# Optimization experiments

Measured on AMD Instinct MI355X. Metric: run time of the kernel, lower is better.

The kernel has to match this reference:

```python
import jax, jax.numpy as jnp
import numpy as np

# dims: E ensemble, F feature channels, O = num_objs+1 nodes, B batch
E, F, O, B, DIN = 4, 16, 9, 512, 32
H, DK = 4, 32          # num_heads, attn_dim per head
DH = 128               # feature_fc / attn_out / post_fc hidden dim
FINAL = F + 1          # final_size = feature_dim + 1


def _lin(x, w, b=None):
    # per-ensemble, per-channel, per-object batched linear:
    # x: [E,F,O,B,i], w: [E,F,O,i,j], b: [E,F,O,1,j]
    y = jnp.einsum('efobi,efoij->efobj', x, w)
    return y if b is None else y + b


def _channel_mha(x, wq, wk, wv, wo, pw, pb):
    # Channel multi-head attention over the O object nodes, per (E,F) channel.
    e, f, o, b, _ = x.shape
    heads = lambda t: t.reshape(e, f, o, b, H, DK)
    q = heads(_lin(x, wq))
    k = heads(_lin(x, wk))
    v = heads(_lin(x, wv))
    scale = jnp.asarray(1.0 / np.sqrt(DK), x.dtype)
    logits = jnp.einsum('efqbhd,efkbhd->efbhqk', q, k) * scale  # [E,F,B,H,O,O]
    attn = jax.nn.softmax(logits, axis=-1)
    out = jnp.einsum('efbhqk,efkbhd->efqbhd', attn, v).reshape(e, f, o, b, H * DK)
    out = _lin(out, wo) + x                 # output projection + residual
    return jax.nn.relu(_lin(out, pw, pb))   # post_fc (post_fc_dims=[DH])


def setup_inputs() -> dict:
    key = jax.random.key(0)
    ks = jax.random.split(key, 32)
    W = lambda k, shape, fan_in: (jax.random.normal(k, shape, jnp.float32)
                                  / np.sqrt(fan_in).astype(np.float32))
    inp = {}
    inp['x'] = jax.random.normal(ks[0], (E, F, O, B, DIN), jnp.float32)
    inp['fw1'] = W(ks[1], (E, F, O, DIN, DH), DIN)
    inp['fb1'] = jnp.zeros((E, F, O, 1, DH), jnp.float32)
    inp['fw2'] = W(ks[2], (E, F, O, DH, DH), DH)
    inp['fb2'] = jnp.zeros((E, F, O, 1, DH), jnp.float32)
    idx = 3
    for i in range(2):
        for n in ('wq', 'wk', 'wv', 'wo', 'pw'):
            inp[f'a{i}_{n}'] = W(ks[idx], (E, F, O, DH, DH), DH)
            idx += 1
        inp[f'a{i}_pb'] = jnp.zeros((E, F, O, 1, DH), jnp.float32)
    inp['pw1'] = W(ks[idx], (E, F, DH, DH), DH); idx += 1
    inp['pb1'] = jnp.zeros((E, F, 1, DH), jnp.float32)
    inp['pw2'] = W(ks[idx], (E, F, DH, FINAL), DH)
    inp['pb2'] = jnp.zeros((E, F, 1, FINAL), jnp.float32)
    return inp


def reference(x, fw1, fb1, fw2, fb2,
              a0_wq, a0_wk, a0_wv, a0_wo, a0_pw, a0_pb,
              a1_wq, a1_wk, a1_wv, a1_wo, a1_pw, a1_pb,
              pw1, pb1, pw2, pb2):
    # sa_feature per-object MLP (feature_fc_dims = [128, 128])
    h = jax.nn.relu(_lin(x, fw1, fb1))
    h = jax.nn.relu(_lin(h, fw2, fb2))
    # num_attns = 2 ChannelMHAttention blocks over object nodes
    h = _channel_mha(h, a0_wq, a0_wk, a0_wv, a0_wo, a0_pw, a0_pb)
    h = _channel_mha(h, a1_wq, a1_wk, a1_wv, a1_wo, a1_pw, a1_pb)
    # pool over object axis (predictor weights have no object dim)
    pooled = h.mean(axis=2)  # [E,F,B,DH]
    p = jax.nn.relu(jnp.einsum('efbi,efij->efbj', pooled, pw1) + pb1)
    return jnp.einsum('efbi,efij->efbj', p, pw2) + pb2  # [E,F,B,F+1]
```

## Files before the change

### kernel.cpp

```cpp
#include <hip/hip_runtime.h>
#include <hip/hip_bf16.h>

typedef __bf16 bvec8 __attribute__((ext_vector_type(8)));
typedef __bf16 bvec4 __attribute__((ext_vector_type(4)));
typedef float fvec4 __attribute__((ext_vector_type(4)));

#define E_ 4
#define F_ 16
#define O_ 9
#define B_ 512
#define DIN_ 32
#define H_ 4
#define DK_ 32
#define DH_ 128
#define FINAL_ 17
#define EF_ 64
#define EFO_ 576

__global__ __launch_bounds__(256) void transpose_k(const float* __restrict__ in,
                                                   __bf16* __restrict__ out, int R, int C) {
  __shared__ float tile[64 * 65];
  int r0 = blockIdx.y * 64, c0 = blockIdx.x * 64;
  const float* src = in + (size_t)blockIdx.z * R * C;
  __bf16* dst = out + (size_t)blockIdx.z * R * C;
  for (int idx = threadIdx.x; idx < 4096; idx += 256) {
    int r = idx >> 6, c = idx & 63;
    if ((r0 + r) < R && (c0 + c) < C)
      tile[r * 65 + c] = src[(size_t)(r0 + r) * C + (c0 + c)];
  }
  __syncthreads();
  for (int idx = threadIdx.x; idx < 4096; idx += 256) {
    int c = idx >> 6, r = idx & 63;
    if ((r0 + r) < R && (c0 + c) < C)
      dst[(size_t)(c0 + c) * R + (r0 + r)] = (__bf16)tile[r * 65 + c];
  }
}

__global__ __launch_bounds__(256) void transpose3_k(const float* __restrict__ i0,
    const float* __restrict__ i1, const float* __restrict__ i2,
    __bf16* __restrict__ o0, __bf16* __restrict__ o1, __bf16* __restrict__ o2) {
  __shared__ float tile[64 * 65];
  int z = blockIdx.z;
  int which = z / EFO_, zb = z - which * EFO_;
  const float* in = which == 0 ? i0 : (which == 1 ? i1 : i2);
  __bf16* out = which == 0 ? o0 : (which == 1 ? o1 : o2);
  int r0 = blockIdx.y * 64, c0 = blockIdx.x * 64;
  const float* src = in + (size_t)zb * DH_ * DH_;
  __bf16* dst = out + (size_t)zb * DH_ * DH_;
  for (int idx = threadIdx.x; idx < 4096; idx += 256) {
    int r = idx >> 6, c = idx & 63;
    tile[r * 65 + c] = src[(size_t)(r0 + r) * DH_ + (c0 + c)];
  }
  __syncthreads();
  for (int idx = threadIdx.x; idx < 4096; idx += 256) {
    int c = idx >> 6, r = idx & 63;
    dst[(size_t)(c0 + c) * DH_ + (r0 + r)] = (__bf16)tile[r * 65 + c];
  }
}

__global__ __launch_bounds__(256) void transpose2_k(const float* __restrict__ i0,
    const float* __restrict__ i1, __bf16* __restrict__ o0, __bf16* __restrict__ o1) {
  __shared__ float tile[64 * 65];
  int z = blockIdx.z;
  int which = z / EFO_, zb = z - which * EFO_;
  const float* in = which == 0 ? i0 : i1;
  __bf16* out = which == 0 ? o0 : o1;
  int r0 = blockIdx.y * 64, c0 = blockIdx.x * 64;
  const float* src = in + (size_t)zb * DH_ * DH_;
  __bf16* dst = out + (size_t)zb * DH_ * DH_;
  for (int idx = threadIdx.x; idx < 4096; idx += 256) {
    int r = idx >> 6, c = idx & 63;
    tile[r * 65 + c] = src[(size_t)(r0 + r) * DH_ + (c0 + c)];
  }
  __syncthreads();
  for (int idx = threadIdx.x; idx < 4096; idx += 256) {
    int c = idx >> 6, r = idx & 63;
    dst[(size_t)(c0 + c) * DH_ + (r0 + r)] = (__bf16)tile[r * 65 + c];
  }
}


__device__ __forceinline__ void stage_async(const __bf16* __restrict__ g, int ldg,
                                            __bf16* s, int cols) {
  int lane = threadIdx.x & 63, w = threadIdx.x >> 6;
  int nwb = cols >> 2;
  for (int wb = w; wb < nwb; wb += 8) {
    int p = wb >> 3, r0 = (wb & 7) << 4;
    int r = r0 + (lane >> 2), c = lane & 3;
    const __bf16* gp = g + (size_t)r * ldg + p * 32 + c * 8;
    __bf16* lp = s + (((p << 7) + r0) << 5);
    __builtin_amdgcn_global_load_lds((const __attribute__((address_space(1))) void*)gp,
                                     (__attribute__((address_space(3))) void*)lp,
                                     16, 0, 0);
  }
}

__device__ __forceinline__ void stage_tile_f32_512(const float* __restrict__ g, int ldg,
                                                   __bf16* s, int cols) {
  int cpr = cols >> 3;
  int nch = 128 * cpr;
  for (int c = threadIdx.x; c < nch; c += 512) {
    int r = c / cpr;
    int cc = (c - r * cpr) << 3;
    const float* gp = g + (size_t)r * ldg + cc;
    float4 f0 = *(const float4*)gp;
    float4 f1 = *(const float4*)(gp + 4);
    bvec8 bv;
    bv[0] = (__bf16)f0.x; bv[1] = (__bf16)f0.y; bv[2] = (__bf16)f0.z; bv[3] = (__bf16)f0.w;
    bv[4] = (__bf16)f1.x; bv[5] = (__bf16)f1.y; bv[6] = (__bf16)f1.z; bv[7] = (__bf16)f1.w;
    *(bvec8*)(s + ((cc >> 5) * 128 + r) * 32 + (cc & 31)) = bv;
  }
}

__device__ __forceinline__ void stage_tile(const __bf16* __restrict__ g, int ldg,
                                           __bf16* s, int cols) {
  int cpr = cols >> 3;
  int nch = 128 * cpr;
  for (int c = threadIdx.x; c < nch; c += 256) {
    int r = c / cpr;
    int cc = (c - r * cpr) << 3;
    *(uint4*)(s + ((cc >> 5) * 128 + r) * 32 + (cc & 31)) =
        *(const uint4*)(g + (size_t)r * ldg + cc);
  }
}

__device__ __forceinline__ void gemm128_8(const __bf16* Ms, const __bf16* Ns, int K,
                                          fvec4 acc[4][2], int wm, int wn, int lm, int q8) {
  for (int k0 = 0; k0 < K; k0 += 32) {
    const __bf16* ap = Ms + (k0 >> 5) * 4096 + q8;
    const __bf16* bp = Ns + (k0 >> 5) * 4096 + q8;
    bvec8 a[4], b[2];
#pragma unroll
    for (int i = 0; i < 4; i++) a[i] = *(const bvec8*)(ap + (wm + i * 16 + lm) * 32);
#pragma unroll
    for (int j = 0; j < 2; j++) b[j] = *(const bvec8*)(bp + (wn + j * 16 + lm) * 32);
#pragma unroll
    for (int i = 0; i < 4; i++)
#pragma unroll
      for (int j = 0; j < 2; j++)
        acc[i][j] = __builtin_amdgcn_mfma_f32_16x16x32_bf16(a[i], b[j], acc[i][j], 0, 0, 0);
  }
}

__device__ __forceinline__ void gemm128(const __bf16* As, const __bf16* Ws, int K,
                                        fvec4 acc[4][4], int wm, int wn, int lm, int q8) {
  for (int k0 = 0; k0 < K; k0 += 32) {
    const __bf16* ap = As + (k0 >> 5) * 4096 + q8;
    const __bf16* bp = Ws + (k0 >> 5) * 4096 + q8;
    bvec8 a[4], b[4];
#pragma unroll
    for (int i = 0; i < 4; i++) a[i] = *(const bvec8*)(ap + (wm + i * 16 + lm) * 32);
#pragma unroll
    for (int j = 0; j < 4; j++) b[j] = *(const bvec8*)(bp + (wn + j * 16 + lm) * 32);
#pragma unroll
    for (int i = 0; i < 4; i++)
#pragma unroll
      for (int j = 0; j < 4; j++)
        acc[i][j] = __builtin_amdgcn_mfma_f32_16x16x32_bf16(a[i], b[j], acc[i][j], 0, 0, 0);
  }
}

__global__ __launch_bounds__(512) void mlp_kernel(const float* __restrict__ x,
    const __bf16* __restrict__ fw1t, const float* __restrict__ fb1,
    const __bf16* __restrict__ fw2t, const float* __restrict__ fb2,
    __bf16* __restrict__ h0) {
  __shared__ __align__(16) __bf16 smem[32768];
  int efo = blockIdx.y, mt = blockIdx.x;
  int t = threadIdx.x, l = t & 63, w = t >> 6;
  int wm = (w & 1) * 64, wn = (w >> 1) * 32;
  int lm = l & 15, q8 = (l >> 4) * 8, qr = (l >> 4) * 4;
  __bf16* xs = smem;
  __bf16* w1s = smem + 4096;
  __bf16* h1s = smem;
  __bf16* w2s = smem + 16384;
  stage_async(fw2t + (size_t)efo * DH_ * DH_, DH_, w2s, DH_);
  stage_async(fw1t + (size_t)efo * DH_ * DIN_, DIN_, w1s, DIN_);
  stage_tile_f32_512(x + ((size_t)efo * B_ + mt * 128) * DIN_, DIN_, xs, DIN_);
  __syncthreads();
  fvec4 zero4 = {0.f, 0.f, 0.f, 0.f};
  fvec4 acc[4][2];
#pragma unroll
  for (int i = 0; i < 4; i++)
#pragma unroll
    for (int j = 0; j < 2; j++) acc[i][j] = zero4;
  gemm128_8(w1s, xs, 32, acc, wm, wn, lm, q8);
  __syncthreads();
#pragma unroll
  for (int i = 0; i < 4; i++) {
    float4 b4 = *(const float4*)(fb1 + efo * DH_ + wm + i * 16 + qr);
    float br[4] = {b4.x, b4.y, b4.z, b4.w};
#pragma unroll
    for (int j = 0; j < 2; j++) {
      int wc0 = wm + i * 16 + qr, bb = wn + j * 16 + lm;
      bvec4 pk;
#pragma unroll
      for (int r = 0; r < 4; r++) pk[r] = (__bf16)fmaxf(acc[i][j][r] + br[r], 0.f);
      *(bvec4*)(h1s + ((wc0 >> 5) * 128 + bb) * 32 + (wc0 & 31)) = pk;
    }
  }
  __syncthreads();
#pragma unroll
  for (int i = 0; i < 4; i++)
#pragma unroll
    for (int j = 0; j < 2; j++) acc[i][j] = zero4;
  gemm128_8(w2s, h1s, 128, acc, wm, wn, lm, q8);
#pragma unroll
  for (int i = 0; i < 4; i++) {
    float4 b4 = *(const float4*)(fb2 + efo * DH_ + wm + i * 16 + qr);
    float br[4] = {b4.x, b4.y, b4.z, b4.w};
#pragma unroll
    for (int j = 0; j < 2; j++) {
      int wc0 = wm + i * 16 + qr, bb = wn + j * 16 + lm;
      bvec4 pk;
#pragma unroll
      for (int r = 0; r < 4; r++) pk[r] = (__bf16)fmaxf(acc[i][j][r] + br[r], 0.f);
      *(bvec4*)(h0 + ((size_t)efo * B_ + mt * 128 + bb) * DH_ + wc0) = pk;
    }
  }
}

__global__ __launch_bounds__(512) void qkv_kernel(const __bf16* __restrict__ hsrc,
    const __bf16* __restrict__ wqt, const __bf16* __restrict__ wkt,
    const __bf16* __restrict__ wvt, __bf16* __restrict__ qdst,
    __bf16* __restrict__ kdst, __bf16* __restrict__ vdst) {
  __shared__ __align__(16) __bf16 smem[32768];
  int efo = blockIdx.y, mt = blockIdx.x;
  int ef = efo / O_, o = efo - ef * O_;
  int t = threadIdx.x, l = t & 63, w = t >> 6;
  int wm = (w & 1) * 64, wn = (w >> 1) * 32;
  int lm = l & 15, q8 = (l >> 4) * 8, qr = (l >> 4) * 4;
  __bf16* hs = smem;
  __bf16* wsm = smem + 16384;
  stage_async(hsrc + ((size_t)efo * B_ + mt * 128) * DH_, DH_, hs, DH_);
  stage_async(wqt + (size_t)efo * DH_ * DH_, DH_, wsm, DH_);
  fvec4 zero4 = {0.f, 0.f, 0.f, 0.f};
  fvec4 acc[4][2];
  auto zero_acc = [&]() {
#pragma unroll
    for (int i = 0; i < 4; i++)
#pragma unroll
      for (int j = 0; j < 2; j++) acc[i][j] = zero4;
  };
  auto store_head = [&](__bf16* __restrict__ dst) {
#pragma unroll
    for (int i = 0; i < 4; i++)
#pragma unroll
      for (int j = 0; j < 2; j++) {
        int wc0 = wm + i * 16 + qr, bb = wn + j * 16 + lm;
        bvec4 pk;
#pragma unroll
        for (int r = 0; r < 4; r++) pk[r] = (__bf16)acc[i][j][r];
        *(bvec4*)(dst + ((((size_t)ef * H_ + (wc0 >> 5)) * O_ + o) * B_ +
                         mt * 128 + bb) * DK_ + (wc0 & 31)) = pk;
      }
  };
  __syncthreads();
  zero_acc();
  gemm128_8(wsm, hs, 128, acc, wm, wn, lm, q8);
  __syncthreads();
  stage_async(wkt + (size_t)efo * DH_ * DH_, DH_, wsm, DH_);
  store_head(qdst);
  __syncthreads();
  zero_acc();
  gemm128_8(wsm, hs, 128, acc, wm, wn, lm, q8);
  __syncthreads();
  stage_async(wvt + (size_t)efo * DH_ * DH_, DH_, wsm, DH_);
  store_head(kdst);
  __syncthreads();
  zero_acc();
  gemm128_8(wsm, hs, 128, acc, wm, wn, lm, q8);
  store_head(vdst);
}

__global__ __launch_bounds__(256) void attn_kernel(const __bf16* __restrict__ q,
    __bf16* kv, const __bf16* __restrict__ v) {
  int t = threadIdx.x;
  int g = t >> 2, sub = t & 3;
  int blk = blockIdx.x;
  int bt = blk & 7, efh = blk >> 3;
  int b = bt * 64 + g, d0 = sub * 8;
  size_t base = (size_t)efh * O_ * B_ * DK_ + (size_t)b * DK_ + d0;
  const size_t ostr = (size_t)B_ * DK_;
  bvec8 kr[9], vr[9];
#pragma unroll
  for (int o = 0; o < 9; o++) kr[o] = *(const bvec8*)(kv + base + (size_t)o * ostr);
#pragma unroll
  for (int o = 0; o < 9; o++) vr[o] = *(const bvec8*)(v + base + (size_t)o * ostr);
  const float scale = 0.17677669529663687f;
#pragma unroll 1
  for (int oq = 0; oq < 9; oq++) {
    bvec8 qv = *(const bvec8*)(q + base + (size_t)oq * ostr);
    float qf[8];
#pragma unroll
    for (int j = 0; j < 8; j++) qf[j] = (float)qv[j];
    float lg[9];
#pragma unroll
    for (int ok = 0; ok < 9; ok++) {
      float s = 0.f;
#pragma unroll
      for (int j = 0; j < 8; j++) s += qf[j] * (float)kr[ok][j];
      s += __shfl_xor(s, 1);
      s += __shfl_xor(s, 2);
      lg[ok] = s * scale;
    }
    float mx = lg[0];
#pragma unroll
    for (int ok = 1; ok < 9; ok++) mx = fmaxf(mx, lg[ok]);
    float sum = 0.f;
#pragma unroll
    for (int ok = 0; ok < 9; ok++) { lg[ok] = __expf(lg[ok] - mx); sum += lg[ok]; }
    float inv = 1.f / sum;
    float oacc[8] = {0.f, 0.f, 0.f, 0.f, 0.f, 0.f, 0.f, 0.f};
#pragma unroll
    for (int ok = 0; ok < 9; ok++)
#pragma unroll
      for (int j = 0; j < 8; j++) oacc[j] += lg[ok] * (float)vr[ok][j];
    bvec8 ov;
#pragma unroll
    for (int j = 0; j < 8; j++) ov[j] = (__bf16)(oacc[j] * inv);
    *(bvec8*)(kv + base + (size_t)oq * ostr) = ov;
  }
}

__global__ __launch_bounds__(512) void proj_kernel(const __bf16* __restrict__ ain,
    const __bf16* __restrict__ wot, const __bf16* __restrict__ pwt,
    const float* __restrict__ pb, const __bf16* resid,
    __bf16* hout) {
  __shared__ __align__(16) __bf16 smem[32768];
  int efo = blockIdx.y, mt = blockIdx.x;
  int ef = efo / O_, o = efo - ef * O_;
  int t = threadIdx.x, l = t & 63, w = t >> 6;
  int wm = (w & 1) * 64, wn = (w >> 1) * 32;
  int lm = l & 15, q8 = (l >> 4) * 8, qr = (l >> 4) * 4;
  __bf16* as2 = smem;
  __bf16* wsm = smem + 16384;
#pragma unroll
  for (int hh = 0; hh < 4; hh++)
    stage_async(ain + ((((size_t)ef * H_ + hh) * O_ + o) * B_ + mt * 128) * DK_, DK_,
                as2 + hh * 4096, DK_);
  stage_async(wot + (size_t)efo * DH_ * DH_, DH_, wsm, DH_);
  __syncthreads();
  fvec4 zero4 = {0.f, 0.f, 0.f, 0.f};
  fvec4 acc[4][2];
#pragma unroll
  for (int i = 0; i < 4; i++)
#pragma unroll
    for (int j = 0; j < 2; j++) acc[i][j] = zero4;
  gemm128_8(wsm, as2, 128, acc, wm, wn, lm, q8);
#pragma unroll
  for (int i = 0; i < 4; i++)
#pragma unroll
    for (int j = 0; j < 2; j++) {
      int wc0 = wm + i * 16 + qr, bb = wn + j * 16 + lm;
      bvec4 rv = *(const bvec4*)(resid + ((size_t)efo * B_ + mt * 128 + bb) * DH_ + wc0);
#pragma unroll
      for (int r = 0; r < 4; r++) acc[i][j][r] += (float)rv[r];
    }
  __syncthreads();
  stage_async(pwt + (size_t)efo * DH_ * DH_, DH_, wsm, DH_);
#pragma unroll
  for (int i = 0; i < 4; i++)
#pragma unroll
    for (int j = 0; j < 2; j++) {
      int wc0 = wm + i * 16 + qr, bb = wn + j * 16 + lm;
      bvec4 pk;
#pragma unroll
      for (int r = 0; r < 4; r++) pk[r] = (__bf16)acc[i][j][r];
      *(bvec4*)(as2 + ((wc0 >> 5) * 128 + bb) * 32 + (wc0 & 31)) = pk;
    }
  __syncthreads();
#pragma unroll
  for (int i = 0; i < 4; i++)
#pragma unroll
    for (int j = 0; j < 2; j++) acc[i][j] = zero4;
  gemm128_8(wsm, as2, 128, acc, wm, wn, lm, q8);
#pragma unroll
  for (int i = 0; i < 4; i++) {
    float4 b4 = *(const float4*)(pb + efo * DH_ + wm + i * 16 + qr);
    float br[4] = {b4.x, b4.y, b4.z, b4.w};
#pragma unroll
    for (int j = 0; j < 2; j++) {
      int wc0 = wm + i * 16 + qr, bb = wn + j * 16 + lm;
      bvec4 pk;
#pragma unroll
      for (int r = 0; r < 4; r++) pk[r] = (__bf16)fmaxf(acc[i][j][r] + br[r], 0.f);
      *(bvec4*)(hout + ((size_t)efo * B_ + mt * 128 + bb) * DH_ + wc0) = pk;
    }
  }
}

__global__ __launch_bounds__(256) void pool_kernel(const __bf16* __restrict__ h2,
                                                   __bf16* __restrict__ pooled) {
  size_t idx = ((size_t)blockIdx.x * 256 + threadIdx.x) * 8;
  int ef = (int)(idx >> 16);
  int rem = (int)(idx & 65535);
  float accv[8] = {0.f, 0.f, 0.f, 0.f, 0.f, 0.f, 0.f, 0.f};
#pragma unroll
  for (int o = 0; o < 9; o++) {
    bvec8 tv = *(const bvec8*)(h2 + (size_t)(ef * O_ + o) * B_ * DH_ + rem);
#pragma unroll
    for (int j = 0; j < 8; j++) accv[j] += (float)tv[j];
  }
  const float inv9 = 1.f / 9.f;
  bvec8 ov;
#pragma unroll
  for (int j = 0; j < 8; j++) ov[j] = (__bf16)(accv[j] * inv9);
  *(bvec8*)(pooled + idx) = ov;
}

__global__ __launch_bounds__(256) void pred_kernel(const __bf16* __restrict__ pooled,
    const __bf16* __restrict__ pw1t, const float* __restrict__ pb1,
    const __bf16* __restrict__ pw2t, const float* __restrict__ pb2,
    float* __restrict__ out) {
  __shared__ __align__(16) __bf16 smem[32768];
  int ef = blockIdx.y, mt = blockIdx.x;
  int t = threadIdx.x, l = t & 63, w = t >> 6;
  int wm = (w & 1) * 64, wn = (w >> 1) * 64;
  int lm = l & 15, q8 = (l >> 4) * 8, qr = (l >> 4) * 4;
  __bf16* ps = smem;
  __bf16* wsm = smem + 16384;
  stage_tile(pooled + ((size_t)ef * B_ + mt * 128) * DH_, DH_, ps, DH_);
  stage_tile(pw1t + (size_t)ef * DH_ * DH_, DH_, wsm, DH_);
  __syncthreads();
  fvec4 zero4 = {0.f, 0.f, 0.f, 0.f};
  fvec4 acc[4][4];
#pragma unroll
  for (int i = 0; i < 4; i++)
#pragma unroll
    for (int j = 0; j < 4; j++) acc[i][j] = zero4;
  gemm128(ps, wsm, 128, acc, wm, wn, lm, q8);
  __syncthreads();
  float bias[4];
#pragma unroll
  for (int j = 0; j < 4; j++) bias[j] = pb1[ef * DH_ + wn + j * 16 + lm];
#pragma unroll
  for (int i = 0; i < 4; i++)
#pragma unroll
    for (int j = 0; j < 4; j++)
#pragma unroll
      for (int r = 0; r < 4; r++) {
        float vv = fmaxf(acc[i][j][r] + bias[j], 0.f);
        int row = wm + i * 16 + qr + r, col = wn + j * 16 + lm;
        ps[((col >> 5) * 128 + row) * 32 + (col & 31)] = (__bf16)vv;
      }
  for (int c = threadIdx.x; c < 512; c += 256) {
    int r = c >> 4, cc = (c & 15) << 3;
    uint4 val;
    val.x = val.y = val.z = val.w = 0u;
    if (r < FINAL_)
      val = *(const uint4*)(pw2t + (size_t)ef * FINAL_ * DH_ + r * DH_ + cc);
    *(uint4*)(wsm + ((cc >> 5) * 32 + r) * 32 + (cc & 31)) = val;
  }
  __syncthreads();
  fvec4 acc2[2][2];
#pragma unroll
  for (int i = 0; i < 2; i++)
#pragma unroll
    for (int j = 0; j < 2; j++) acc2[i][j] = zero4;
  for (int k0 = 0; k0 < 128; k0 += 32) {
    bvec8 a2[2], b2[2];
#pragma unroll
    for (int i = 0; i < 2; i++)
      a2[i] = *(const bvec8*)(ps + ((k0 >> 5) * 128 + w * 32 + i * 16 + lm) * 32 + q8);
#pragma unroll
    for (int j = 0; j < 2; j++)
      b2[j] = *(const bvec8*)(wsm + ((k0 >> 5) * 32 + j * 16 + lm) * 32 + q8);
#pragma unroll
    for (int i = 0; i < 2; i++)
#pragma unroll
      for (int j = 0; j < 2; j++)
        acc2[i][j] = __builtin_amdgcn_mfma_f32_16x16x32_bf16(a2[i], b2[j], acc2[i][j], 0, 0, 0);
  }
#pragma unroll
  for (int i = 0; i < 2; i++)
#pragma unroll
    for (int j = 0; j < 2; j++)
#pragma unroll
      for (int r = 0; r < 4; r++) {
        int col = j * 16 + lm;
        if (col < FINAL_) {
          int b = mt * 128 + w * 32 + i * 16 + qr + r;
          out[((size_t)ef * B_ + b) * FINAL_ + col] =
              acc2[i][j][r] + pb2[ef * FINAL_ + col];
        }
      }
}

extern "C" void kernel_launch(void* const* d_in, const int* in_sizes, int n_in,
                              void* d_out, int out_size, void* d_ws, size_t ws_size,
                              hipStream_t stream) {
  (void)in_sizes; (void)n_in; (void)out_size; (void)ws_size;
  const float* x     = (const float*)d_in[0];
  const float* fb1   = (const float*)d_in[2];
  const float* fb2   = (const float*)d_in[4];
  const float* a0_pb = (const float*)d_in[10];
  const float* a1_pb = (const float*)d_in[16];
  const float* pb1   = (const float*)d_in[18];
  const float* pb2   = (const float*)d_in[20];

  __bf16* wsb = (__bf16*)d_ws;
  const size_t SLOT = (size_t)EFO_ * DH_ * DH_;
  const size_t ABUF = (size_t)EFO_ * B_ * DH_;
  __bf16* s0 = wsb;
  __bf16* s1 = s0 + SLOT;
  __bf16* s2 = s1 + SLOT;
  __bf16* A0 = s2 + SLOT;
  __bf16* A1 = A0 + ABUF;
  __bf16* A2 = A1 + ABUF;
  __bf16* A3 = A2 + ABUF;

  auto T = [&](const void* src, __bf16* dst, int R, int C, int batch) {
    dim3 g((C + 63) / 64, (R + 63) / 64, batch);
    transpose_k<<<g, 256, 0, stream>>>((const float*)src, dst, R, C);
  };

  dim3 gg(4, EFO_);

  T(d_in[1], s0, DIN_, DH_, EFO_);
  T(d_in[3], s1, DH_, DH_, EFO_);
  mlp_kernel<<<gg, 512, 0, stream>>>(x, s0, fb1, s1, fb2, A0);

  for (int blkI = 0; blkI < 2; blkI++) {
    int wbase = blkI == 0 ? 5 : 11;
    const float* pb = blkI == 0 ? a0_pb : a1_pb;
    transpose3_k<<<dim3(2, 2, EFO_ * 3), 256, 0, stream>>>(
        (const float*)d_in[wbase], (const float*)d_in[wbase + 1],
        (const float*)d_in[wbase + 2], s0, s1, s2);
    qkv_kernel<<<gg, 512, 0, stream>>>(A0, s0, s1, s2, A1, A2, A3);
    attn_kernel<<<2048, 256, 0, stream>>>(A1, A2, A3);
    transpose2_k<<<dim3(2, 2, EFO_ * 2), 256, 0, stream>>>(
        (const float*)d_in[wbase + 3], (const float*)d_in[wbase + 4], s0, s1);
    proj_kernel<<<gg, 512, 0, stream>>>(A2, s0, s1, pb, A0, A0);
  }

  T(d_in[17], s0, DH_, DH_, EF_);
  T(d_in[19], s1, DH_, FINAL_, EF_);
  pool_kernel<<<2048, 256, 0, stream>>>(A0, s2);
  pred_kernel<<<dim3(4, EF_), 256, 0, stream>>>(s2, s0, pb1, s1, pb2,
                                                (float*)d_out);
}
```

Before: 1.014 ms.

## Fuse weight transpose and bf16 conversion into GEMM kernels, remap blocks to XCDs

Removes the separate transpose kernels for the MLP, QKV, projection and predictor weights. Each GEMM kernel now reads the fp32 weights directly, transposes them through registers, converts to bf16 and writes them to LDS. Weight loads are overlapped with output stores where possible. A 1D grid with XCD-aware block decoding places the four batch tiles of one efo on the same XCD so they share L2 for the weight reads. The cost is that each of the four tiles re-reads and re-converts the fp32 weights with strided column loads instead of async LDS loads of pre-transposed bf16.

```diff
diff --git a/kernel.cpp b/kernel.cpp
--- a/kernel.cpp
+++ b/kernel.cpp
@@ -36,47 +36,11 @@
   }
 }
 
-__global__ __launch_bounds__(256) void transpose3_k(const float* __restrict__ i0,
-    const float* __restrict__ i1, const float* __restrict__ i2,
-    __bf16* __restrict__ o0, __bf16* __restrict__ o1, __bf16* __restrict__ o2) {
-  __shared__ float tile[64 * 65];
-  int z = blockIdx.z;
-  int which = z / EFO_, zb = z - which * EFO_;
-  const float* in = which == 0 ? i0 : (which == 1 ? i1 : i2);
-  __bf16* out = which == 0 ? o0 : (which == 1 ? o1 : o2);
-  int r0 = blockIdx.y * 64, c0 = blockIdx.x * 64;
-  const float* src = in + (size_t)zb * DH_ * DH_;
-  __bf16* dst = out + (size_t)zb * DH_ * DH_;
-  for (int idx = threadIdx.x; idx < 4096; idx += 256) {
-    int r = idx >> 6, c = idx & 63;
-    tile[r * 65 + c] = src[(size_t)(r0 + r) * DH_ + (c0 + c)];
-  }
-  __syncthreads();
-  for (int idx = threadIdx.x; idx < 4096; idx += 256) {
-    int c = idx >> 6, r = idx & 63;
-    dst[(size_t)(c0 + c) * DH_ + (r0 + r)] = (__bf16)tile[r * 65 + c];
-  }
-}
-
-__global__ __launch_bounds__(256) void transpose2_k(const float* __restrict__ i0,
-    const float* __restrict__ i1, __bf16* __restrict__ o0, __bf16* __restrict__ o1) {
-  __shared__ float tile[64 * 65];
-  int z = blockIdx.z;
-  int which = z / EFO_, zb = z - which * EFO_;
-  const float* in = which == 0 ? i0 : i1;
-  __bf16* out = which == 0 ? o0 : o1;
-  int r0 = blockIdx.y * 64, c0 = blockIdx.x * 64;
-  const float* src = in + (size_t)zb * DH_ * DH_;
-  __bf16* dst = out + (size_t)zb * DH_ * DH_;
-  for (int idx = threadIdx.x; idx < 4096; idx += 256) {
-    int r = idx >> 6, c = idx & 63;
-    tile[r * 65 + c] = src[(size_t)(r0 + r) * DH_ + (c0 + c)];
-  }
-  __syncthreads();
-  for (int idx = threadIdx.x; idx < 4096; idx += 256) {
-    int c = idx >> 6, r = idx & 63;
-    dst[(size_t)(c0 + c) * DH_ + (r0 + r)] = (__bf16)tile[r * 65 + c];
-  }
+__device__ __forceinline__ void decode_id(int& efo, int& mt) {
+  int id = blockIdx.x;
+  int xcd = id & 7, wi = id >> 3;
+  efo = xcd * 72 + (wi >> 2);
+  mt = wi & 3;
 }
 
 
@@ -92,6 +56,57 @@
     __builtin_amdgcn_global_load_lds((const __attribute__((address_space(1))) void*)gp,
                                      (__attribute__((address_space(3))) void*)lp,
                                      16, 0, 0);
+  }
+}
+
+template <int K>
+__device__ __forceinline__ void stage_wT_load(const float* __restrict__ g,
+                                              float regs[][8]) {
+  int t = threadIdx.x, l = t & 63;
+  int slot = l >> 4;
+  int j = (t >> 6) * 16 + (l & 15);
+#pragma unroll
+  for (int gi = 0; gi < K / 32; gi++) {
+    int i0 = (4 * gi + slot) * 8;
+#pragma unroll
+    for (int r = 0; r < 8; r++)
+      regs[gi][r] = g[(size_t)(i0 + r) * 128 + j];
+  }
+}
+template <int K>
+__device__ __forceinline__ void stage_wT_write(const float regs[][8], __bf16* s) {
+  int t = threadIdx.x, l = t & 63;
+  int slot = l >> 4;
+  int j = (t >> 6) * 16 + (l & 15);
+#pragma unroll
+  for (int gi = 0; gi < K / 32; gi++) {
+    bvec8 bv;
+#pragma unroll
+    for (int r = 0; r < 8; r++) bv[r] = (__bf16)regs[gi][r];
+    *(bvec8*)(s + (gi * 128 + j) * 32 + slot * 8) = bv;
+  }
+}
+
+__device__ __forceinline__ void stage_wT_256(const float* __restrict__ g, __bf16* s) {
+  int t = threadIdx.x, l = t & 63;
+  int slot = l >> 4;
+  int jb = (t >> 6) * 16 + (l & 15);
+#pragma unroll
+  for (int jh = 0; jh < 2; jh++) {
+    int j = jh * 64 + jb;
+    float regs[4][8];
+#pragma unroll
+    for (int gi = 0; gi < 4; gi++)
+#pragma unroll
+      for (int r = 0; r < 8; r++)
+        regs[gi][r] = g[(size_t)((4 * gi + slot) * 8 + r) * 128 + j];
+#pragma unroll
+    for (int gi = 0; gi < 4; gi++) {
+      bvec8 bv;
+#pragma unroll
+      for (int r = 0; r < 8; r++) bv[r] = (__bf16)regs[gi][r];
+      *(bvec8*)(s + (gi * 128 + j) * 32 + slot * 8) = bv;
+    }
   }
 }
 
@@ -161,11 +176,12 @@
 }
 
 __global__ __launch_bounds__(512) void mlp_kernel(const float* __restrict__ x,
-    const __bf16* __restrict__ fw1t, const float* __restrict__ fb1,
-    const __bf16* __restrict__ fw2t, const float* __restrict__ fb2,
+    const float* __restrict__ fw1, const float* __restrict__ fb1,
+    const float* __restrict__ fw2, const float* __restrict__ fb2,
     __bf16* __restrict__ h0) {
   __shared__ __align__(16) __bf16 smem[32768];
-  int efo = blockIdx.y, mt = blockIdx.x;
+  int efo, mt;
+  decode_id(efo, mt);
   int t = threadIdx.x, l = t & 63, w = t >> 6;
   int wm = (w & 1) * 64, wn = (w >> 1) * 32;
   int lm = l & 15, q8 = (l >> 4) * 8, qr = (l >> 4) * 4;
@@ -173,9 +189,12 @@
   __bf16* w1s = smem + 4096;
   __bf16* h1s = smem;
   __bf16* w2s = smem + 16384;
-  stage_async(fw2t + (size_t)efo * DH_ * DH_, DH_, w2s, DH_);
-  stage_async(fw1t + (size_t)efo * DH_ * DIN_, DIN_, w1s, DIN_);
+  float r1[1][8], r2[4][8];
+  stage_wT_load<32>(fw1 + (size_t)efo * DH_ * DIN_, r1);
+  stage_wT_load<128>(fw2 + (size_t)efo * DH_ * DH_, r2);
   stage_tile_f32_512(x + ((size_t)efo * B_ + mt * 128) * DIN_, DIN_, xs, DIN_);
+  stage_wT_write<32>(r1, w1s);
+  stage_wT_write<128>(r2, w2s);
   __syncthreads();
   fvec4 zero4 = {0.f, 0.f, 0.f, 0.f};
   fvec4 acc[4][2];
@@ -220,19 +239,23 @@
 }
 
 __global__ __launch_bounds__(512) void qkv_kernel(const __bf16* __restrict__ hsrc,
-    const __bf16* __restrict__ wqt, const __bf16* __restrict__ wkt,
-    const __bf16* __restrict__ wvt, __bf16* __restrict__ qdst,
+    const float* __restrict__ wq, const float* __restrict__ wk,
+    const float* __restrict__ wv, __bf16* __restrict__ qdst,
     __bf16* __restrict__ kdst, __bf16* __restrict__ vdst) {
   __shared__ __align__(16) __bf16 smem[32768];
-  int efo = blockIdx.y, mt = blockIdx.x;
+  int efo, mt;
+  decode_id(efo, mt);
   int ef = efo / O_, o = efo - ef * O_;
   int t = threadIdx.x, l = t & 63, w = t >> 6;
   int wm = (w & 1) * 64, wn = (w >> 1) * 32;
   int lm = l & 15, q8 = (l >> 4) * 8, qr = (l >> 4) * 4;
   __bf16* hs = smem;
   __bf16* wsm = smem + 16384;
+  size_t wofs = (size_t)efo * DH_ * DH_;
   stage_async(hsrc + ((size_t)efo * B_ + mt * 128) * DH_, DH_, hs, DH_);
-  stage_async(wqt + (size_t)efo * DH_ * DH_, DH_, wsm, DH_);
+  float rw[4][8];
+  stage_wT_load<128>(wq + wofs, rw);
+  stage_wT_write<128>(rw, wsm);
   fvec4 zero4 = {0.f, 0.f, 0.f, 0.f};
   fvec4 acc[4][2];
   auto zero_acc = [&]() {
@@ -258,14 +281,16 @@
   zero_acc();
   gemm128_8(wsm, hs, 128, acc, wm, wn, lm, q8);
   __syncthreads();
-  stage_async(wkt + (size_t)efo * DH_ * DH_, DH_, wsm, DH_);
+  stage_wT_load<128>(wk + wofs, rw);
   store_head(qdst);
+  stage_wT_write<128>(rw, wsm);
   __syncthreads();
   zero_acc();
   gemm128_8(wsm, hs, 128, acc, wm, wn, lm, q8);
   __syncthreads();
-  stage_async(wvt + (size_t)efo * DH_ * DH_, DH_, wsm, DH_);
+  stage_wT_load<128>(wv + wofs, rw);
   store_head(kdst);
+  stage_wT_write<128>(rw, wsm);
   __syncthreads();
   zero_acc();
   gemm128_8(wsm, hs, 128, acc, wm, wn, lm, q8);
@@ -323,22 +348,26 @@
 }
 
 __global__ __launch_bounds__(512) void proj_kernel(const __bf16* __restrict__ ain,
-    const __bf16* __restrict__ wot, const __bf16* __restrict__ pwt,
+    const float* __restrict__ wo, const float* __restrict__ pw,
     const float* __restrict__ pb, const __bf16* resid,
     __bf16* hout) {
   __shared__ __align__(16) __bf16 smem[32768];
-  int efo = blockIdx.y, mt = blockIdx.x;
+  int efo, mt;
+  decode_id(efo, mt);
   int ef = efo / O_, o = efo - ef * O_;
   int t = threadIdx.x, l = t & 63, w = t >> 6;
   int wm = (w & 1) * 64, wn = (w >> 1) * 32;
   int lm = l & 15, q8 = (l >> 4) * 8, qr = (l >> 4) * 4;
   __bf16* as2 = smem;
   __bf16* wsm = smem + 16384;
+  size_t wofs = (size_t)efo * DH_ * DH_;
 #pragma unroll
   for (int hh = 0; hh < 4; hh++)
     stage_async(ain + ((((size_t)ef * H_ + hh) * O_ + o) * B_ + mt * 128) * DK_, DK_,
                 as2 + hh * 4096, DK_);
-  stage_async(wot + (size_t)efo * DH_ * DH_, DH_, wsm, DH_);
+  float rw[4][8];
+  stage_wT_load<128>(wo + wofs, rw);
+  stage_wT_write<128>(rw, wsm);
   __syncthreads();
   fvec4 zero4 = {0.f, 0.f, 0.f, 0.f};
   fvec4 acc[4][2];
@@ -357,7 +386,7 @@
       for (int r = 0; r < 4; r++) acc[i][j][r] += (float)rv[r];
     }
   __syncthreads();
-  stage_async(pwt + (size_t)efo * DH_ * DH_, DH_, wsm, DH_);
+  stage_wT_load<128>(pw + wofs, rw);
 #pragma unroll
   for (int i = 0; i < 4; i++)
 #pragma unroll
@@ -368,6 +397,7 @@
       for (int r = 0; r < 4; r++) pk[r] = (__bf16)acc[i][j][r];
       *(bvec4*)(as2 + ((wc0 >> 5) * 128 + bb) * 32 + (wc0 & 31)) = pk;
     }
+  stage_wT_write<128>(rw, wsm);
   __syncthreads();
 #pragma unroll
   for (int i = 0; i < 4; i++)
@@ -409,7 +439,7 @@
 }
 
 __global__ __launch_bounds__(256) void pred_kernel(const __bf16* __restrict__ pooled,
-    const __bf16* __restrict__ pw1t, const float* __restrict__ pb1,
+    const float* __restrict__ pw1, const float* __restrict__ pb1,
     const __bf16* __restrict__ pw2t, const float* __restrict__ pb2,
     float* __restrict__ out) {
   __shared__ __align__(16) __bf16 smem[32768];
@@ -420,7 +450,7 @@
   __bf16* ps = smem;
   __bf16* wsm = smem + 16384;
   stage_tile(pooled + ((size_t)ef * B_ + mt * 128) * DH_, DH_, ps, DH_);
-  stage_tile(pw1t + (size_t)ef * DH_ * DH_, DH_, wsm, DH_);
+  stage_wT_256(pw1 + (size_t)ef * DH_ * DH_, wsm);
   __syncthreads();
   fvec4 zero4 = {0.f, 0.f, 0.f, 0.f};
   fvec4 acc[4][4];
@@ -491,51 +521,44 @@
                               hipStream_t stream) {
   (void)in_sizes; (void)n_in; (void)out_size; (void)ws_size;
   const float* x     = (const float*)d_in[0];
+  const float* fw1   = (const float*)d_in[1];
   const float* fb1   = (const float*)d_in[2];
+  const float* fw2   = (const float*)d_in[3];
   const float* fb2   = (const float*)d_in[4];
   const float* a0_pb = (const float*)d_in[10];
   const float* a1_pb = (const float*)d_in[16];
+  const float* pw1   = (const float*)d_in[17];
   const float* pb1   = (const float*)d_in[18];
   const float* pb2   = (const float*)d_in[20];
 
   __bf16* wsb = (__bf16*)d_ws;
   const size_t SLOT = (size_t)EFO_ * DH_ * DH_;
   const size_t ABUF = (size_t)EFO_ * B_ * DH_;
-  __bf16* s0 = wsb;
-  __bf16* s1 = s0 + SLOT;
+  __bf16* s1 = wsb;
   __bf16* s2 = s1 + SLOT;
   __bf16* A0 = s2 + SLOT;
   __bf16* A1 = A0 + ABUF;
   __bf16* A2 = A1 + ABUF;
   __bf16* A3 = A2 + ABUF;
 
-  auto T = [&](const void* src, __bf16* dst, int R, int C, int batch) {
-    dim3 g((C + 63) / 64, (R + 63) / 64, batch);
-    transpose_k<<<g, 256, 0, stream>>>((const float*)src, dst, R, C);
-  };
-
-  dim3 gg(4, EFO_);
-
-  T(d_in[1], s0, DIN_, DH_, EFO_);
-  T(d_in[3], s1, DH_, DH_, EFO_);
-  mlp_kernel<<<gg, 512, 0, stream>>>(x, s0, fb1, s1, fb2, A0);
+  mlp_kernel<<<2304, 512, 0, stream>>>(x, fw1, fb1, fw2, fb2, A0);
 
   for (int blkI = 0; blkI < 2; blkI++) {
     int wbase = blkI == 0 ? 5 : 11;
     const float* pb = blkI == 0 ? a0_pb : a1_pb;
-    transpose3_k<<<dim3(2, 2, EFO_ * 3), 256, 0, stream>>>(
-        (const float*)d_in[wbase], (const float*)d_in[wbase + 1],
-        (const float*)d_in[wbase + 2], s0, s1, s2);
-    qkv_kernel<<<gg, 512, 0, stream>>>(A0, s0, s1, s2, A1, A2, A3);
+    qkv_kernel<<<2304, 512, 0, stream>>>(A0, (const float*)d_in[wbase],
+                                         (const float*)d_in[wbase + 1],
+                                         (const float*)d_in[wbase + 2], A1, A2, A3);
     attn_kernel<<<2048, 256, 0, stream>>>(A1, A2, A3);
-    transpose2_k<<<dim3(2, 2, EFO_ * 2), 256, 0, stream>>>(
-        (const float*)d_in[wbase + 3], (const float*)d_in[wbase + 4], s0, s1);
-    proj_kernel<<<gg, 512, 0, stream>>>(A2, s0, s1, pb, A0, A0);
-  }
-
-  T(d_in[17], s0, DH_, DH_, EF_);
-  T(d_in[19], s1, DH_, FINAL_, EF_);
+    proj_kernel<<<2304, 512, 0, stream>>>(A2, (const float*)d_in[wbase + 3],
+                                          (const float*)d_in[wbase + 4], pb, A0, A0);
+  }
+
+  {
+    dim3 g((FINAL_ + 63) / 64, (DH_ + 63) / 64, EF_);
+    transpose_k<<<g, 256, 0, stream>>>((const float*)d_in[19], s1, DH_, FINAL_);
+  }
   pool_kernel<<<2048, 256, 0, stream>>>(A0, s2);
-  pred_kernel<<<dim3(4, EF_), 256, 0, stream>>>(s2, s0, pb1, s1, pb2,
+  pred_kernel<<<dim3(4, EF_), 256, 0, stream>>>(s2, pw1, pb1, s1, pb2,
                                                 (float*)d_out);
 }
```

Measured after the change: 897.4 us. 1.13x faster.
